# Performance work log

Hardware: AMD Instinct MI355X
Metric: run time of the kernel (lower is better)

The kernel has to match this reference:

```python
import jax, jax.numpy as jnp
import numpy as np

S_LEN = 8        # stride_length
LEVELS = 4       # corr_levels
RADIUS = 3       # corr_radius
CD = 2 * RADIUS + 1  # corr_dim = 7
PLANES = ((0, 1), (0, 2), (1, 2))  # itertools.combinations(range(3), 2)


def _bilinear(img, pts):
    # img: (C,H,W); pts: (...,2) normalized [-1,1], x->W, y->H; align_corners=True, border padding
    C, H, W = img.shape
    x = jnp.clip((pts[..., 0] + 1.0) * 0.5 * (W - 1), 0.0, W - 1.0)
    y = jnp.clip((pts[..., 1] + 1.0) * 0.5 * (H - 1), 0.0, H - 1.0)
    x0f = jnp.floor(x); y0f = jnp.floor(y)
    x0 = x0f.astype(jnp.int32); y0 = y0f.astype(jnp.int32)
    x1 = jnp.minimum(x0 + 1, W - 1); y1 = jnp.minimum(y0 + 1, H - 1)
    wx = x - x0f; wy = y - y0f
    return (img[:, y0, x0] * (1 - wy) * (1 - wx) + img[:, y0, x1] * (1 - wy) * wx
            + img[:, y1, x0] * wy * (1 - wx) + img[:, y1, x1] * wy * wx)


def _trilinear(vol, pts):
    # vol: (C,D,H,W); pts: (...,3) normalized, x->W, y->H, z->D; align_corners=True, border padding
    C, D, H, W = vol.shape
    x = jnp.clip((pts[..., 0] + 1.0) * 0.5 * (W - 1), 0.0, W - 1.0)
    y = jnp.clip((pts[..., 1] + 1.0) * 0.5 * (H - 1), 0.0, H - 1.0)
    z = jnp.clip((pts[..., 2] + 1.0) * 0.5 * (D - 1), 0.0, float(max(D - 1, 0)))
    x0f = jnp.floor(x); y0f = jnp.floor(y); z0f = jnp.floor(z)
    x0 = x0f.astype(jnp.int32); y0 = y0f.astype(jnp.int32); z0 = z0f.astype(jnp.int32)
    x1 = jnp.minimum(x0 + 1, W - 1); y1 = jnp.minimum(y0 + 1, H - 1); z1 = jnp.minimum(z0 + 1, D - 1)
    wx = x - x0f; wy = y - y0f; wz = z - z0f
    out = (vol[:, z0, y0, x0] * (1 - wz) * (1 - wy) * (1 - wx)
           + vol[:, z0, y0, x1] * (1 - wz) * (1 - wy) * wx
           + vol[:, z0, y1, x0] * (1 - wz) * wy * (1 - wx)
           + vol[:, z0, y1, x1] * (1 - wz) * wy * wx
           + vol[:, z1, y0, x0] * wz * (1 - wy) * (1 - wx)
           + vol[:, z1, y0, x1] * wz * (1 - wy) * wx
           + vol[:, z1, y1, x0] * wz * wy * (1 - wx)
           + vol[:, z1, y1, x1] * wz * wy * wx)
    return out


def setup_inputs():
    key = jax.random.key(0)
    ks = jax.random.split(key, 5)
    B, N, V, DLAT = 1, 256, 96, 128
    coords = jax.random.uniform(ks[0], (B, S_LEN, N, 3), jnp.float32) * (V - 1)
    coords_init = jax.random.uniform(ks[1], (B, N, 3), jnp.float32) * (V - 1)
    feature_planes = jax.random.normal(ks[2], (B * S_LEN, DLAT * 3, V, V), jnp.float32)
    w1 = jax.random.normal(ks[3], (CD ** 4, 384), jnp.float32) * 0.02
    b1 = jnp.zeros((384,), jnp.float32)
    w2 = jax.random.normal(ks[4], (384, 256), jnp.float32) * 0.05
    b2 = jnp.zeros((256,), jnp.float32)
    return dict(coords=coords, coords_init=coords_init, feature_planes=feature_planes,
                w1=w1, b1=b1, w2=w2, b2=b2)


def _forward(coords, coords_init, feature_planes, w1, b1, w2, b2):
    B, S, N, _ = coords.shape
    dt = coords.dtype
    off = jnp.arange(CD, dtype=dt) - RADIUS
    oc = jnp.stack(jnp.meshgrid(off, off, indexing='ij'), -1)        # (7,7,2) spatial offsets
    oc3 = jnp.concatenate([oc, jnp.zeros_like(oc[..., :1])], -1)     # (7,7,3) zero time offset
    # ---- init_levels: feature pyramid + initial track features ----
    fp = feature_planes  # ((B S), (D*3), V, V)
    fplevels, tflevels = [], []
    for i in range(LEVELS):
        if i > 0:
            bs, c, v, _ = fp.shape
            fp = fp.reshape(bs, c, v // 2, 2, v // 2, 2).mean(axis=(3, 5))  # avg_pool2d(2,2)
        bs, c, v, _ = fp.shape
        d = c // 3
        lev = fp.reshape(B, S, d, 3, v, v).transpose(0, 1, 2, 4, 5, 3)  # (B,S,d,v,v,planes)
        fplevels.append(lev)
        scale3 = jnp.array([v - 1, v - 1, S - 1], dt)
        # time coordinate = batch index (faithful to get_track_features t construction)
        t = jnp.broadcast_to(jnp.arange(B, dtype=dt)[:, None, None], (B, N, 1))
        tfs = []
        for k, (a, b2_) in enumerate(PLANES):
            c3 = jnp.concatenate([coords_init[..., (a, b2_)] / (2.0 ** i), t], -1)  # (B,N,3)
            reg = c3[:, None, None, :, :] + oc3[None, :, :, None, :]  # (B,7,7,N,3)
            g = reg * (2.0 / scale3) - 1.0
            vol = lev[..., k].transpose(0, 2, 1, 3, 4)  # (B,d,S,v,v)
            samp = jax.vmap(_trilinear)(vol, g)          # (B,d,7,7,N)
            tfs.append(samp.reshape(B, d, CD * CD, N).transpose(0, 2, 3, 1))  # (B,49,N,d)
        tflevels.append(jnp.stack(tfs, -1))  # (B,49,N,d,planes)
    # ---- get_corr_features: per-level 4D correlation volumes + corr_mlp ----
    outs = []
    for i in range(LEVELS):
        lev = fplevels[i]
        v = lev.shape[3]; d = lev.shape[2]
        scale2 = jnp.array([v - 1, v - 1], dt)
        acc = None
        for k, (a, b2_) in enumerate(PLANES):
            c2 = (coords[..., (a, b2_)] / (2.0 ** i)).reshape(B * S, N, 2)
            reg = c2[:, :, None, None, :] + oc[None, None, :, :, :]  # (BS,N,7,7,2)
            g = reg * (2.0 / scale2) - 1.0
            frames = lev[..., k].reshape(B * S, d, v, v)
            cf2 = jax.vmap(_bilinear)(frames, g)                     # (BS,d,N,7,7)
            cf2 = cf2.transpose(0, 2, 3, 4, 1).reshape(B, S, N, CD, CD, d)  # b s n h w d
            tf = tflevels[i][..., k].transpose(0, 2, 3, 1).reshape(B, N, d, CD, CD)  # b n d x y
            c4 = jnp.einsum('bsnhwd,bndxy->bsnhwxy', cf2, tf).reshape(B * S * N, CD ** 4)
            h = jax.nn.gelu(c4 @ w1 + b1, approximate=True)
            o = h @ w2 + b2
            acc = o if acc is None else acc + o
        outs.append(acc)
    return jnp.concatenate(outs, -1).reshape(B, S, N, LEVELS * w2.shape[1])


def reference(coords, coords_init, feature_planes, w1, b1, w2, b2):
    return _forward(coords, coords_init, feature_planes, w1, b1, w2, b2)
```

## Files before the change

kernel.cpp:

```cpp
#include <hip/hip_runtime.h>
#include <hip/hip_bf16.h>
#include <math.h>

#define NTRK 256
#define DLAT 128
#define CDIM 7
#define CD2  49
#define CD4  2401
#define NH1  384
#define NH2  256
#define LDK  2432
#define PITCHB 272

#define SZ_L0 ((size_t)3 * 8 * 96 * 96 * 128)
#define SZ_L1 ((size_t)3 * 8 * 48 * 48 * 128)
#define SZ_L2 ((size_t)3 * 8 * 24 * 24 * 128)
#define SZ_L3 ((size_t)3 * 8 * 12 * 12 * 128)
#define SZ_TF ((size_t)3 * NTRK * DLAT * CD2)

typedef __attribute__((ext_vector_type(8))) short short8;
typedef __attribute__((ext_vector_type(4))) float f32x4;
typedef __attribute__((ext_vector_type(4))) unsigned int u32x4;


__device__ __forceinline__ float b2f(unsigned short u) {
    union { unsigned int i; float f; } c;
    c.i = ((unsigned int)u) << 16;
    return c.f;
}
__device__ __forceinline__ unsigned int f2b(float x) {
    __hip_bfloat16 h = __float2bfloat16(x);
    return (unsigned int)(*(unsigned short*)&h);
}

__device__ __forceinline__ float gelu_tanh(float x) {
    float x2 = x * x;
    float p = x * fmaf(0.044715f, x2, 1.0f);
    float e = __expf(-1.5957691216f * p);
    return __fdividef(x, 1.0f + e);
}

__device__ __forceinline__ int plane_a(int k) { return (k == 2) ? 1 : 0; }
__device__ __forceinline__ int plane_b(int k) { return (k == 0) ? 1 : 2; }

__device__ __forceinline__ int lev_v(int lev) { return 96 >> lev; }
__device__ __forceinline__ size_t lev_off(int lev) {
    return (lev > 0 ? SZ_L0 : 0) + (lev > 1 ? SZ_L1 : 0) + (lev > 2 ? SZ_L2 : 0);
}

__device__ __forceinline__ void gload16(const void* g, void* l) {
    __builtin_amdgcn_global_load_lds(
        (const __attribute__((address_space(1))) unsigned int*)g,
        (__attribute__((address_space(3))) unsigned int*)l,
        16, 0, 0);
}


__global__ __launch_bounds__(256) void cvt_cl_kernel(const float* __restrict__ in,
                                                     __hip_bfloat16* __restrict__ out) {
    __shared__ unsigned int lds[64][97];
    const int b = blockIdx.x;
    const int y = b % 96;
    const int ks = b / 96;
    const int k = ks >> 3, s = ks & 7;
    const int tid = threadIdx.x;
    for (int idx = tid; idx < 64 * 24; idx += 256) {
        int d2 = idx / 24, x4 = (idx - d2 * 24) * 4;
        const float* rlo = in + (((size_t)s * 384 + (2 * d2) * 3 + k) * 96 + y) * 96 + x4;
        const float* rhi = in + (((size_t)s * 384 + (2 * d2 + 1) * 3 + k) * 96 + y) * 96 + x4;
        float4 lo = *(const float4*)rlo;
        float4 hi = *(const float4*)rhi;
        lds[d2][x4 + 0] = f2b(lo.x) | (f2b(hi.x) << 16);
        lds[d2][x4 + 1] = f2b(lo.y) | (f2b(hi.y) << 16);
        lds[d2][x4 + 2] = f2b(lo.z) | (f2b(hi.z) << 16);
        lds[d2][x4 + 3] = f2b(lo.w) | (f2b(hi.w) << 16);
    }
    __syncthreads();
    unsigned int* orow = (unsigned int*)((unsigned short*)out + ((size_t)ks * 96 + y) * 96 * 128);
    for (int idx = tid; idx < 96 * 16; idx += 256) {
        int x = idx >> 4, q = idx & 15;
        u32x4 r;
        r[0] = lds[4 * q + 0][x];
        r[1] = lds[4 * q + 1][x];
        r[2] = lds[4 * q + 2][x];
        r[3] = lds[4 * q + 3][x];
        *(u32x4*)(orow + x * 64 + q * 4) = r;
    }
}


__global__ __launch_bounds__(256) void pool_cl(const __hip_bfloat16* __restrict__ in,
                                               __hip_bfloat16* __restrict__ out,
                                               int vin, int total8) {
    int idx = blockIdx.x * 256 + threadIdx.x;
    if (idx >= total8) return;
    int vout = vin >> 1;
    int d8 = idx & 15;
    int t = idx >> 4;
    int x = t % vout; t /= vout;
    int y = t % vout; t /= vout;
    const unsigned short* base = (const unsigned short*)in
        + (((size_t)t * vin + 2 * y) * vin + 2 * x) * 128 + d8 * 8;
    short8 a = *(const short8*)(base);
    short8 bq = *(const short8*)(base + 128);
    short8 c = *(const short8*)(base + (size_t)vin * 128);
    short8 d = *(const short8*)(base + (size_t)vin * 128 + 128);
    short8 r;
    #pragma unroll
    for (int j = 0; j < 8; ++j) {
        float sum = b2f((unsigned short)a[j]) + b2f((unsigned short)bq[j])
                  + b2f((unsigned short)c[j]) + b2f((unsigned short)d[j]);
        r[j] = (short)f2b(0.25f * sum);
    }
    *(short8*)((unsigned short*)out + ((((size_t)t * vout + y) * vout + x)) * 128 + d8 * 8) = r;
}


__global__ __launch_bounds__(256) void tf_all(const __hip_bfloat16* __restrict__ levbase,
                                              const float* __restrict__ coords_init,
                                              __hip_bfloat16* __restrict__ tfb) {
    const int bid = blockIdx.x;
    const int lev = bid / 768;
    const int r0 = bid - lev * 768;
    const int g = (r0 & 7) * 96 + (r0 >> 3);
    const int k = g >> 8;
    const int n = g & 255;
    const int v = lev_v(lev);
    const float inv_scale = 1.f / (float)(1 << lev);
    const float vm1 = (float)(v - 1);
    float cx = coords_init[n * 3 + plane_a(k)] * inv_scale;
    float cy = coords_init[n * 3 + plane_b(k)] * inv_scale;
    const unsigned short* frame = (const unsigned short*)levbase + lev_off(lev)
        + (size_t)(k * 8) * v * v * 128;
    unsigned short* dst = (unsigned short*)tfb + (size_t)lev * SZ_TF
        + ((size_t)(k * NTRK + n)) * (DLAT * CD2);
    for (int idx = threadIdx.x; idx < CD2 * 16; idx += 256) {
        int xy = idx >> 4;
        int c8 = idx & 15;
        int i = xy / CDIM, j = xy % CDIM;
        float X = fminf(fmaxf(cx + (float)(i - 3), 0.f), vm1);
        float Y = fminf(fmaxf(cy + (float)(j - 3), 0.f), vm1);
        float xf = floorf(X), yf = floorf(Y);
        int x0 = (int)xf, y0 = (int)yf;
        int x1 = min(x0 + 1, v - 1), y1 = min(y0 + 1, v - 1);
        float wx = X - xf, wy = Y - yf;
        const unsigned short* r00 = frame + ((size_t)y0 * v + x0) * 128 + c8 * 8;
        const unsigned short* r01 = frame + ((size_t)y0 * v + x1) * 128 + c8 * 8;
        const unsigned short* r10 = frame + ((size_t)y1 * v + x0) * 128 + c8 * 8;
        const unsigned short* r11 = frame + ((size_t)y1 * v + x1) * 128 + c8 * 8;
        short8 a = *(const short8*)r00, bq = *(const short8*)r01;
        short8 c = *(const short8*)r10, d = *(const short8*)r11;
        float w00 = (1.f - wy) * (1.f - wx), w01 = (1.f - wy) * wx;
        float w10 = wy * (1.f - wx), w11 = wy * wx;
        short8 r;
        #pragma unroll
        for (int e = 0; e < 8; ++e) {
            float val = b2f((unsigned short)a[e]) * w00 + b2f((unsigned short)bq[e]) * w01
                      + b2f((unsigned short)c[e]) * w10 + b2f((unsigned short)d[e]) * w11;
            r[e] = (short)f2b(val);
        }
        *(short8*)(dst + xy * 128 + c8 * 8) = r;
    }
}


__global__ __launch_bounds__(256) void corr_all(const __hip_bfloat16* __restrict__ levbase,
                                                const float* __restrict__ coords,
                                                const __hip_bfloat16* __restrict__ tfb,
                                                __hip_bfloat16* __restrict__ c4b) {
    __shared__ __align__(16) char patch[64 * PITCHB];
    __shared__ __align__(16) char tfs[64 * PITCHB];
    __shared__ float wxs[8], wys[8];
    const int bid = blockIdx.x;
    const int lk = bid >> 8;
    const int n = bid & 255;
    const int lev = lk / 3;
    const int k = lk - lev * 3;
    const int v = lev_v(lev);
    const int vv = v * v;
    const float inv_scale = 1.f / (float)(1 << lev);
    const int tid = threadIdx.x;
    const float vm1 = (float)(v - 1);

    const short8* tfg = (const short8*)(tfb + (size_t)lev * SZ_TF
        + ((size_t)(k * NTRK + n)) * (DLAT * CD2));
    for (int idx = tid; idx < 784; idx += 256) {
        int row = idx >> 4, c16 = idx & 15;
        *(short8*)(tfs + row * PITCHB + c16 * 16) = tfg[idx];
    }

    const int hwb = tid / 49;
    const int xy  = tid - hwb * 49;
    const bool act = tid < 245;

    const unsigned short* fbase = (const unsigned short*)levbase + lev_off(lev)
        + (size_t)(k * 8) * vv * 128;
    const int w4 = tid >> 6, l = tid & 63;
    const int l15 = l & 15, l4 = l >> 4;

    for (int s = 0; s < 8; ++s) {
        const int sn = s * 256 + n;
        float cx = coords[sn * 3 + plane_a(k)] * inv_scale;
        float cy = coords[sn * 3 + plane_b(k)] * inv_scale;
        const int fx = (int)floorf(cx), fy = (int)floorf(cy);

        if (tid < 7) {
            float X = fminf(fmaxf(cx + (float)(tid - 3), 0.f), vm1);
            int g = min(max(fx + tid - 3, 0), v - 1);
            wxs[tid] = X - (float)g;
            float Y = fminf(fmaxf(cy + (float)(tid - 3), 0.f), vm1);
            int gy_ = min(max(fy + tid - 3, 0), v - 1);
            wys[tid] = Y - (float)gy_;
        }
        {
            const unsigned short* frame = fbase + (size_t)s * vv * 128;
            for (int idx = tid; idx < 1024; idx += 256) {
                int pos = idx >> 4, c8 = idx & 15;
                int px = pos & 7, py = pos >> 3;
                int gx = min(max(fx + px - 3, 0), v - 1);
                int gy = min(max(fy + py - 3, 0), v - 1);
                *(short8*)(patch + pos * PITCHB + c8 * 16) =
                    *(const short8*)(frame + ((size_t)gy * v + gx) * 128 + c8 * 8);
            }
        }
        __syncthreads();

        f32x4 acc[4];
        #pragma unroll
        for (int nt = 0; nt < 4; ++nt) acc[nt] = (f32x4){0.f, 0.f, 0.f, 0.f};
        #pragma unroll
        for (int ks = 0; ks < 4; ++ks) {
            short8 af = *(const short8*)(patch + (16 * w4 + l15) * PITCHB + ks * 64 + l4 * 16);
            #pragma unroll
            for (int nt = 0; nt < 4; ++nt) {
                short8 bf = *(const short8*)(tfs + (16 * nt + l15) * PITCHB + ks * 64 + l4 * 16);
                acc[nt] = __builtin_amdgcn_mfma_f32_16x16x32_bf16(af, bf, acc[nt], 0, 0, 0);
            }
        }
        __syncthreads();

        {
            const int row0 = 16 * w4 + l4 * 4;
            #pragma unroll
            for (int nt = 0; nt < 4; ++nt) {
                int col = nt * 16 + l15;
                #pragma unroll
                for (int j = 0; j < 4; ++j)
                    *(float*)(patch + (row0 + j) * PITCHB + col * 4) = acc[nt][j];
            }
        }
        __syncthreads();

        unsigned short* crow = (unsigned short*)c4b + ((size_t)lk * 2048 + sn) * LDK;
        if (act) {
            int h = 0, w = hwb;
            unsigned short* op = crow + tid;
            const char* colbase = patch + xy * 4;
            #pragma unroll
            for (int it = 0; it < 10; ++it) {
                if (h < 7) {
                    float wxv = wxs[h], wyv = wys[w];
                    const char* tap = colbase + (w * 8 + h) * PITCHB;
                    float p00 = *(const float*)(tap);
                    float p01 = *(const float*)(tap + PITCHB);
                    float p10 = *(const float*)(tap + 8 * PITCHB);
                    float p11 = *(const float*)(tap + 9 * PITCHB);
                    float a  = fmaf(wxv, p01 - p00, p00);
                    float bq = fmaf(wxv, p11 - p10, p10);
                    *op = (unsigned short)f2b(fmaf(wyv, bq - a, a));
                }
                w += 5; if (w >= 7) { w -= 7; h += 1; }
                op += 245;
            }
        }
        if (tid < LDK - CD4) crow[CD4 + tid] = 0;
        __syncthreads();
    }
}


__global__ __launch_bounds__(256) void prep_w1t(const float* __restrict__ w1,
                                                __hip_bfloat16* __restrict__ w1t) {
    int idx = blockIdx.x * 256 + threadIdx.x;
    if (idx >= NH1 * LDK) return;
    int n = idx / LDK, kk = idx - n * LDK;
    float v = (kk < CD4) ? w1[(size_t)kk * NH1 + n] : 0.f;
    w1t[idx] = __float2bfloat16(v);
}

__global__ __launch_bounds__(256) void prep_w2t(const float* __restrict__ w2,
                                                __hip_bfloat16* __restrict__ w2t) {
    int idx = blockIdx.x * 256 + threadIdx.x;
    if (idx >= NH2 * NH1) return;
    int n = idx / NH1, j = idx - n * NH1;
    w2t[idx] = __float2bfloat16(w2[(size_t)j * NH2 + n]);
}


__global__ __launch_bounds__(256) void gemm1_all(
    const __hip_bfloat16* __restrict__ A,
    const __hip_bfloat16* __restrict__ Bt,
    const float* __restrict__ b1,
    __hip_bfloat16* __restrict__ H) {
    __shared__ __align__(16) char smem[16384];
    char* Asm = smem;
    char* Bsm = smem + 8192;
    const int m0 = blockIdx.x * 128, n0 = blockIdx.y * 128;
    const int tid = threadIdx.x;
    const int w = tid >> 6, l = tid & 63;
    const int wr = w >> 1, wc = w & 1;
    const int l15 = l & 15, l4 = l >> 4;
    f32x4 acc[4][4];
    #pragma unroll
    for (int m = 0; m < 4; ++m)
        #pragma unroll
        for (int n = 0; n < 4; ++n) acc[m][n] = (f32x4){0.f, 0.f, 0.f, 0.f};
    const char* Ag = (const char*)(A + (size_t)(m0 + (tid >> 2)) * LDK) + (tid & 3) * 16;
    const char* Bg = (const char*)(Bt + (size_t)(n0 + (tid >> 2)) * LDK) + (tid & 3) * 16;
    char* AsmW = Asm + w * 1024;
    char* BsmW = Bsm + w * 1024;
    for (int kb = 0; kb < LDK * 2; kb += 64) {
        gload16(Ag + kb, AsmW);
        gload16(Ag + (size_t)64 * LDK * 2 + kb, AsmW + 4096);
        gload16(Bg + kb, BsmW);
        gload16(Bg + (size_t)64 * LDK * 2 + kb, BsmW + 4096);
        __syncthreads();
        short8 af[4], bfr[4];
        #pragma unroll
        for (int m = 0; m < 4; ++m)
            af[m] = *(const short8*)(Asm + (wr * 64 + m * 16 + l15) * 64 + l4 * 16);
        #pragma unroll
        for (int n = 0; n < 4; ++n)
            bfr[n] = *(const short8*)(Bsm + (wc * 64 + n * 16 + l15) * 64 + l4 * 16);
        #pragma unroll
        for (int m = 0; m < 4; ++m)
            #pragma unroll
            for (int n = 0; n < 4; ++n)
                acc[m][n] = __builtin_amdgcn_mfma_f32_16x16x32_bf16(af[m], bfr[n], acc[m][n], 0, 0, 0);
        __syncthreads();
    }
    #pragma unroll
    for (int m = 0; m < 4; ++m) {
        int row = m0 + wr * 64 + m * 16 + l4 * 4;
        #pragma unroll
        for (int n = 0; n < 4; ++n) {
            int col = n0 + wc * 64 + n * 16 + l15;
            float bias = b1[col];
            #pragma unroll
            for (int j = 0; j < 4; ++j)
                H[(size_t)(row + j) * NH1 + col] = __float2bfloat16(gelu_tanh(acc[m][n][j] + bias));
        }
    }
}


__global__ __launch_bounds__(256) void gemm2_all(
    const __hip_bfloat16* __restrict__ Hin,
    const __hip_bfloat16* __restrict__ Bt,
    const float* __restrict__ b2,
    float* __restrict__ out) {
    __shared__ __align__(16) char smem[8192];
    char* Asm = smem;
    char* Bsm = smem + 4096;
    const int lev = blockIdx.x >> 5;
    const int m0 = (blockIdx.x & 31) * 64, n0 = blockIdx.y * 64;
    const int tid = threadIdx.x;
    const int w = tid >> 6, l = tid & 63;
    const int wr = w >> 1, wc = w & 1;
    const int l15 = l & 15, l4 = l >> 4;
    f32x4 acc[2][2];
    #pragma unroll
    for (int m = 0; m < 2; ++m)
        #pragma unroll
        for (int n = 0; n < 2; ++n) acc[m][n] = (f32x4){0.f, 0.f, 0.f, 0.f};
    const char* Bg = (const char*)(Bt + (size_t)(n0 + (tid >> 2)) * NH1) + (tid & 3) * 16;
    char* AsmW = Asm + w * 1024;
    char* BsmW = Bsm + w * 1024;
    for (int p = 0; p < 3; ++p) {
        const char* Ag = (const char*)(Hin
            + (size_t)((lev * 3 + p) * 2048 + m0 + (tid >> 2)) * NH1) + (tid & 3) * 16;
        for (int jb = 0; jb < NH1 * 2; jb += 64) {
            gload16(Ag + jb, AsmW);
            gload16(Bg + jb, BsmW);
            __syncthreads();
            short8 af[2], bfr[2];
            #pragma unroll
            for (int m = 0; m < 2; ++m)
                af[m] = *(const short8*)(Asm + (wr * 32 + m * 16 + l15) * 64 + l4 * 16);
            #pragma unroll
            for (int n = 0; n < 2; ++n)
                bfr[n] = *(const short8*)(Bsm + (wc * 32 + n * 16 + l15) * 64 + l4 * 16);
            #pragma unroll
            for (int m = 0; m < 2; ++m)
                #pragma unroll
                for (int n = 0; n < 2; ++n)
                    acc[m][n] = __builtin_amdgcn_mfma_f32_16x16x32_bf16(af[m], bfr[n], acc[m][n], 0, 0, 0);
            __syncthreads();
        }
    }
    #pragma unroll
    for (int m = 0; m < 2; ++m) {
        int row = m0 + wr * 32 + m * 16 + l4 * 4;
        #pragma unroll
        for (int n = 0; n < 2; ++n) {
            int col = n0 + wc * 32 + n * 16 + l15;
            float bias3 = 3.f * b2[col];
            #pragma unroll
            for (int j = 0; j < 4; ++j)
                out[(size_t)(row + j) * 1024 + lev * NH2 + col] = acc[m][n][j] + bias3;
        }
    }
}


extern "C" void kernel_launch(void* const* d_in, const int* in_sizes, int n_in,
                              void* d_out, int out_size, void* d_ws, size_t ws_size,
                              hipStream_t stream) {
    const float* coords      = (const float*)d_in[0];
    const float* coords_init = (const float*)d_in[1];
    const float* fp0         = (const float*)d_in[2];
    const float* w1          = (const float*)d_in[3];
    const float* b1          = (const float*)d_in[4];
    const float* w2          = (const float*)d_in[5];
    const float* b2          = (const float*)d_in[6];
    float* out = (float*)d_out;
    char* ws = (char*)d_ws;

    __hip_bfloat16* lev0 = (__hip_bfloat16*)ws;      ws += SZ_L0 * 2;
    __hip_bfloat16* lev1 = (__hip_bfloat16*)ws;      ws += SZ_L1 * 2;
    __hip_bfloat16* lev2 = (__hip_bfloat16*)ws;      ws += SZ_L2 * 2;
    __hip_bfloat16* lev3 = (__hip_bfloat16*)ws;      ws += SZ_L3 * 2;
    __hip_bfloat16* tfb  = (__hip_bfloat16*)ws;      ws += (size_t)4 * SZ_TF * 2;
    __hip_bfloat16* c4b  = (__hip_bfloat16*)ws;      ws += (size_t)24576 * LDK * 2;
    __hip_bfloat16* h_ws = (__hip_bfloat16*)ws;      ws += (size_t)24576 * NH1 * 2;
    __hip_bfloat16* w1t  = (__hip_bfloat16*)ws;      ws += (size_t)NH1 * LDK * 2;
    __hip_bfloat16* w2t  = (__hip_bfloat16*)ws;      ws += (size_t)NH2 * NH1 * 2;

    prep_w1t<<<(NH1 * LDK + 255) / 256, 256, 0, stream>>>(w1, w1t);
    prep_w2t<<<(NH2 * NH1 + 255) / 256, 256, 0, stream>>>(w2, w2t);

    cvt_cl_kernel<<<24 * 96, 256, 0, stream>>>(fp0, lev0);
    pool_cl<<<(int)((SZ_L1 / 8 + 255) / 256), 256, 0, stream>>>(lev0, lev1, 96, (int)(SZ_L1 / 8));
    pool_cl<<<(int)((SZ_L2 / 8 + 255) / 256), 256, 0, stream>>>(lev1, lev2, 48, (int)(SZ_L2 / 8));
    pool_cl<<<(int)((SZ_L3 / 8 + 255) / 256), 256, 0, stream>>>(lev2, lev3, 24, (int)(SZ_L3 / 8));

    tf_all<<<4 * 768, 256, 0, stream>>>(lev0, coords_init, tfb);
    corr_all<<<3072, 256, 0, stream>>>(lev0, coords, tfb, c4b);
    gemm1_all<<<dim3(192, 3), 256, 0, stream>>>(c4b, w1t, b1, h_ws);
    gemm2_all<<<dim3(128, 4), 256, 0, stream>>>(h_ws, w2t, b2, out);
}
```

Measured before the change: 263.7 us.

## Prefetch next frame patch into registers during MFMA; tile w1 transpose via LDS

In the correlation kernel, the coordinates and the 8x8x128 feature patch for the next time step are now loaded from global memory into registers while the current step's MFMA work runs. The stores into LDS then happen at the start of the following iteration, which hides the global load latency at the cost of extra registers per thread. Separately, the w1 transpose/convert prep kernel is rewritten as a 64x64 tiled transpose through padded shared memory, so both its reads and writes are coalesced. 38*64=2432 matches LDK, so the padding columns are still zeroed.

```diff
diff --git a/kernel.cpp b/kernel.cpp
--- a/kernel.cpp
+++ b/kernel.cpp
@@ -198,12 +198,35 @@
     const int w4 = tid >> 6, l = tid & 63;
     const int l15 = l & 15, l4 = l >> 4;
 
+    const int c8 = tid & 15;
+    const int posb = tid >> 4;
+
+    float cxc, cyc; int fxc, fyc;
+    short8 pre[4];
+
+    auto CALC = [&](int s) {
+        const int sn = s * 256 + n;
+        cxc = coords[sn * 3 + plane_a(k)] * inv_scale;
+        cyc = coords[sn * 3 + plane_b(k)] * inv_scale;
+        fxc = (int)floorf(cxc);
+        fyc = (int)floorf(cyc);
+    };
+    auto PREF = [&](int s) {
+        const unsigned short* frame = fbase + (size_t)s * vv * 128;
+        #pragma unroll
+        for (int q = 0; q < 4; ++q) {
+            int pos = posb + 16 * q;
+            int px = pos & 7, py = pos >> 3;
+            int gx = min(max(fxc + px - 3, 0), v - 1);
+            int gy = min(max(fyc + py - 3, 0), v - 1);
+            pre[q] = *(const short8*)(frame + ((size_t)gy * v + gx) * 128 + c8 * 8);
+        }
+    };
+
+    CALC(0); PREF(0);
     for (int s = 0; s < 8; ++s) {
-        const int sn = s * 256 + n;
-        float cx = coords[sn * 3 + plane_a(k)] * inv_scale;
-        float cy = coords[sn * 3 + plane_b(k)] * inv_scale;
-        const int fx = (int)floorf(cx), fy = (int)floorf(cy);
-
+        const float cx = cxc, cy = cyc;
+        const int fx = fxc, fy = fyc;
         if (tid < 7) {
             float X = fminf(fmaxf(cx + (float)(tid - 3), 0.f), vm1);
             int g = min(max(fx + tid - 3, 0), v - 1);
@@ -212,17 +235,9 @@
             int gy_ = min(max(fy + tid - 3, 0), v - 1);
             wys[tid] = Y - (float)gy_;
         }
-        {
-            const unsigned short* frame = fbase + (size_t)s * vv * 128;
-            for (int idx = tid; idx < 1024; idx += 256) {
-                int pos = idx >> 4, c8 = idx & 15;
-                int px = pos & 7, py = pos >> 3;
-                int gx = min(max(fx + px - 3, 0), v - 1);
-                int gy = min(max(fy + py - 3, 0), v - 1);
-                *(short8*)(patch + pos * PITCHB + c8 * 16) =
-                    *(const short8*)(frame + ((size_t)gy * v + gx) * 128 + c8 * 8);
-            }
-        }
+        #pragma unroll
+        for (int q = 0; q < 4; ++q)
+            *(short8*)(patch + (posb + 16 * q) * PITCHB + c8 * 16) = pre[q];
         __syncthreads();
 
         f32x4 acc[4];
@@ -237,6 +252,7 @@
                 acc[nt] = __builtin_amdgcn_mfma_f32_16x16x32_bf16(af, bf, acc[nt], 0, 0, 0);
             }
         }
+        if (s < 7) { CALC(s + 1); PREF(s + 1); }
         __syncthreads();
 
         {
@@ -251,7 +267,7 @@
         }
         __syncthreads();
 
-        unsigned short* crow = (unsigned short*)c4b + ((size_t)lk * 2048 + sn) * LDK;
+        unsigned short* crow = (unsigned short*)c4b + ((size_t)lk * 2048 + s * 256 + n) * LDK;
         if (act) {
             int h = 0, w = hwb;
             unsigned short* op = crow + tid;
@@ -281,11 +297,19 @@
 
 __global__ __launch_bounds__(256) void prep_w1t(const float* __restrict__ w1,
                                                 __hip_bfloat16* __restrict__ w1t) {
-    int idx = blockIdx.x * 256 + threadIdx.x;
-    if (idx >= NH1 * LDK) return;
-    int n = idx / LDK, kk = idx - n * LDK;
-    float v = (kk < CD4) ? w1[(size_t)kk * NH1 + n] : 0.f;
-    w1t[idx] = __float2bfloat16(v);
+    __shared__ float t[64][65];
+    const int kk0 = blockIdx.x * 64, n0 = blockIdx.y * 64;
+    const int tid = threadIdx.x;
+    for (int idx = tid; idx < 4096; idx += 256) {
+        int r = idx >> 6, c = idx & 63;
+        int kk = kk0 + r;
+        t[r][c] = (kk < CD4) ? w1[(size_t)kk * NH1 + n0 + c] : 0.f;
+    }
+    __syncthreads();
+    for (int idx = tid; idx < 4096; idx += 256) {
+        int r = idx >> 6, c = idx & 63;
+        w1t[(size_t)(n0 + r) * LDK + kk0 + c] = __float2bfloat16(t[c][r]);
+    }
 }
 
 __global__ __launch_bounds__(256) void prep_w2t(const float* __restrict__ w2,
@@ -436,7 +460,7 @@
     __hip_bfloat16* w1t  = (__hip_bfloat16*)ws;      ws += (size_t)NH1 * LDK * 2;
     __hip_bfloat16* w2t  = (__hip_bfloat16*)ws;      ws += (size_t)NH2 * NH1 * 2;
 
-    prep_w1t<<<(NH1 * LDK + 255) / 256, 256, 0, stream>>>(w1, w1t);
+    prep_w1t<<<dim3(38, 6), 256, 0, stream>>>(w1, w1t);
     prep_w2t<<<(NH2 * NH1 + 255) / 256, 256, 0, stream>>>(w2, w2t);
 
     cvt_cl_kernel<<<24 * 96, 256, 0, stream>>>(fp0, lev0);
```

After: 260.0 us. No clear change (-1.4%).
